# Optimization experiments

Hardware: AMD Instinct MI355X
Metric: run time of the kernel (lower is better)

Reference implementation:

```python
import jax, jax.numpy as jnp
import numpy as np
from jax import lax


def _maxpool_same(x, k):
    # stride-1 max pool with symmetric padding p=(k-1)//2, pad value -inf
    # (matches torch max_pool2d implicit -inf padding)
    p = (k - 1) // 2
    return lax.reduce_window(
        x,
        -jnp.inf,
        lax.max,
        window_dimensions=(1, 1, k, k),
        window_strides=(1, 1, 1, 1),
        padding=[(0, 0), (0, 0), (p, p), (p, p)],
    )


def setup_inputs() -> dict:
    key = jax.random.key(0)
    x = jax.random.normal(key, (16, 256, 64, 64), dtype=jnp.float32)
    return {"x": x}


def reference(x):
    # SPP: concat(x, maxpool5(x), maxpool9(x), maxpool13(x)) along channels
    x1 = _maxpool_same(x, 5)
    x2 = _maxpool_same(x, 9)
    x3 = _maxpool_same(x, 13)
    return jnp.concatenate([x, x1, x2, x3], axis=1)  # [B, 4C, H, W]
```

## Files before the change

### kernel.cpp

```cpp
#include <hip/hip_runtime.h>
#include <math.h>

#define TPB 256
#define W 64
#define H 64
#define LDSW 68

__global__ __launch_bounds__(TPB) void spp_kernel(const float* __restrict__ in,
                                                  float* __restrict__ out) {
    __shared__ __align__(16) float s_in[H * LDSW];
    __shared__ __align__(16) float s_r5[H * LDSW];
    __shared__ __align__(16) float s_r9[H * LDSW];
    __shared__ __align__(16) float s_r13[H * LDSW];

    const int tid = threadIdx.x;
    const int bc  = blockIdx.x;
    const int b   = bc >> 8;
    const int c   = bc & 255;
    const size_t img   = (size_t)bc * (H * W);
    const size_t obase = ((size_t)b * 1024 + c) * (H * W);
    const size_t pstr  = (size_t)256 * H * W;
    const float NEG = -INFINITY;

    {
        const float4* in4 = (const float4*)(in + img);
        #pragma unroll
        for (int i = 0; i < 4; ++i) {
            int idx = tid + TPB * i;
            int y = idx >> 4;
            int q = idx & 15;
            float4 v = in4[idx];
            *(float4*)&s_in[y * LDSW + q * 4] = v;
        }
    }
    __syncthreads();

    {
        const int y  = tid >> 2;
        const int x0 = (tid & 3) << 4;
        float seg[32];
        #pragma unroll
        for (int j = 0; j < 8; ++j) {
            int xs = x0 - 8 + 4 * j;
            float4 v;
            if (xs >= 0 && xs < W) v = *(const float4*)&s_in[y * LDSW + xs];
            else                   v = make_float4(NEG, NEG, NEG, NEG);
            seg[4*j+0] = v.x; seg[4*j+1] = v.y; seg[4*j+2] = v.z; seg[4*j+3] = v.w;
        }
        float r5[24];
        #pragma unroll
        for (int i = 0; i < 24; ++i) {
            float m = seg[i+2];
            m = fmaxf(m, seg[i+3]); m = fmaxf(m, seg[i+4]);
            m = fmaxf(m, seg[i+5]); m = fmaxf(m, seg[i+6]);
            r5[i] = m;
        }
        float r9[16], r13[16];
        #pragma unroll
        for (int i = 0; i < 16; ++i) {
            r9[i]  = fmaxf(r5[i+2], r5[i+6]);
            r13[i] = fmaxf(fmaxf(r5[i], r5[i+4]), r5[i+8]);
        }
        const int base = y * LDSW + x0;
        #pragma unroll
        for (int g = 0; g < 4; ++g) {
            *(float4*)&s_r5 [base + 4*g] = make_float4(r5[4+4*g], r5[5+4*g], r5[6+4*g], r5[7+4*g]);
            *(float4*)&s_r9 [base + 4*g] = make_float4(r9[4*g],  r9[4*g+1],  r9[4*g+2],  r9[4*g+3]);
            *(float4*)&s_r13[base + 4*g] = make_float4(r13[4*g], r13[4*g+1], r13[4*g+2], r13[4*g+3]);
        }
    }
    __syncthreads();

    {
        float4* o4 = (float4*)(out + obase);
        #pragma unroll
        for (int i = 0; i < 4; ++i) {
            int idx = tid + TPB * i;
            int y = idx >> 4;
            int q = idx & 15;
            o4[idx] = *(const float4*)&s_in[y * LDSW + q * 4];
        }
    }

    {
        const int x  = tid & 63;
        const int y0 = (tid >> 6) << 4;

        {
            float cv[20];
            #pragma unroll
            for (int j = 0; j < 20; ++j) {
                int y = y0 - 2 + j;
                cv[j] = (y >= 0 && y < H) ? s_r5[y * LDSW + x] : NEG;
            }
            float* o = out + obase + pstr;
            #pragma unroll
            for (int i = 0; i < 16; ++i) {
                float m = cv[i];
                m = fmaxf(m, cv[i+1]); m = fmaxf(m, cv[i+2]);
                m = fmaxf(m, cv[i+3]); m = fmaxf(m, cv[i+4]);
                o[(y0 + i) * W + x] = m;
            }
        }
        {
            float cv[24];
            #pragma unroll
            for (int j = 0; j < 24; ++j) {
                int y = y0 - 4 + j;
                cv[j] = (y >= 0 && y < H) ? s_r9[y * LDSW + x] : NEG;
            }
            float* o = out + obase + 2 * pstr;
            #pragma unroll
            for (int i = 0; i < 16; ++i) {
                float m = cv[i];
                #pragma unroll
                for (int d = 1; d < 9; ++d) m = fmaxf(m, cv[i+d]);
                o[(y0 + i) * W + x] = m;
            }
        }
        {
            float cv[28];
            #pragma unroll
            for (int j = 0; j < 28; ++j) {
                int y = y0 - 6 + j;
                cv[j] = (y >= 0 && y < H) ? s_r13[y * LDSW + x] : NEG;
            }
            float* o = out + obase + 3 * pstr;
            #pragma unroll
            for (int i = 0; i < 16; ++i) {
                float m = cv[i];
                #pragma unroll
                for (int d = 1; d < 13; ++d) m = fmaxf(m, cv[i+d]);
                o[(y0 + i) * W + x] = m;
            }
        }
    }
}

extern "C" void kernel_launch(void* const* d_in, const int* in_sizes, int n_in,
                              void* d_out, int out_size, void* d_ws, size_t ws_size,
                              hipStream_t stream) {
    const float* x = (const float*)d_in[0];
    float* out = (float*)d_out;
    spp_kernel<<<dim3(4096), dim3(TPB), 0, stream>>>(x, out);
}
```

Measured before the change: 315.3 us.

## Compute pyramid pooling from one horizontal-5 LDS buffer with wave shuffles

The kernel now computes the horizontal 5-wide max directly from global loads using wavefront shuffles, writes the passthrough channel straight from registers, and keeps only one LDS buffer instead of four. The vertical pass builds a prefix tree of pairwise maxima to get the 5, 9 and 13 vertical windows, then finishes the wider horizontal windows with cross-lane shuffles at offsets of 2 and 4, clamping at the image edges. This removes a full LDS staging pass, one barrier and three quarters of the LDS footprint, which should raise occupancy. In exchange it adds shuffle instructions and relies on the max-decomposition identities and edge clamping being correct.

```diff
diff --git a/kernel.cpp b/kernel.cpp
--- a/kernel.cpp
+++ b/kernel.cpp
@@ -8,15 +8,13 @@
 
 __global__ __launch_bounds__(TPB) void spp_kernel(const float* __restrict__ in,
                                                   float* __restrict__ out) {
-    __shared__ __align__(16) float s_in[H * LDSW];
     __shared__ __align__(16) float s_r5[H * LDSW];
-    __shared__ __align__(16) float s_r9[H * LDSW];
-    __shared__ __align__(16) float s_r13[H * LDSW];
 
-    const int tid = threadIdx.x;
-    const int bc  = blockIdx.x;
-    const int b   = bc >> 8;
-    const int c   = bc & 255;
+    const int tid  = threadIdx.x;
+    const int lane = tid & 63;
+    const int bc   = blockIdx.x;
+    const int b    = bc >> 8;
+    const int c    = bc & 255;
     const size_t img   = (size_t)bc * (H * W);
     const size_t obase = ((size_t)b * 1024 + c) * (H * W);
     const size_t pstr  = (size_t)256 * H * W;
@@ -24,115 +22,77 @@
 
     {
         const float4* in4 = (const float4*)(in + img);
+        float4* o4 = (float4*)(out + obase);
+        const int  lm1 = (lane - 1) & 63;
+        const int  lp1 = (lane + 1) & 63;
+        const bool qlo = (lane & 15) == 0;
+        const bool qhi = (lane & 15) == 15;
         #pragma unroll
         for (int i = 0; i < 4; ++i) {
-            int idx = tid + TPB * i;
-            int y = idx >> 4;
-            int q = idx & 15;
+            const int idx = tid + TPB * i;
             float4 v = in4[idx];
-            *(float4*)&s_in[y * LDSW + q * 4] = v;
+            o4[idx] = v;
+            float e0 = __shfl(v.z, lm1, 64);
+            float e1 = __shfl(v.w, lm1, 64);
+            float e6 = __shfl(v.x, lp1, 64);
+            float e7 = __shfl(v.y, lp1, 64);
+            if (qlo) { e0 = NEG; e1 = NEG; }
+            if (qhi) { e6 = NEG; e7 = NEG; }
+            const float e2 = v.x, e3 = v.y, e4 = v.z, e5 = v.w;
+            const float p0 = fmaxf(e0, e1), p1 = fmaxf(e1, e2), p2 = fmaxf(e2, e3);
+            const float p3 = fmaxf(e3, e4), p4 = fmaxf(e4, e5), p5 = fmaxf(e5, e6);
+            float4 r;
+            r.x = fmaxf(fmaxf(p0, p2), e4);
+            r.y = fmaxf(fmaxf(p1, p3), e5);
+            r.z = fmaxf(fmaxf(p2, p4), e6);
+            r.w = fmaxf(fmaxf(p3, p5), e7);
+            const int y = idx >> 4;
+            const int q = idx & 15;
+            *(float4*)&s_r5[y * LDSW + 4 * q] = r;
         }
     }
     __syncthreads();
 
     {
-        const int y  = tid >> 2;
-        const int x0 = (tid & 3) << 4;
-        float seg[32];
+        const int x  = lane;
+        const int y0 = (tid >> 6) << 4;
+        float cv[28];
         #pragma unroll
-        for (int j = 0; j < 8; ++j) {
-            int xs = x0 - 8 + 4 * j;
-            float4 v;
-            if (xs >= 0 && xs < W) v = *(const float4*)&s_in[y * LDSW + xs];
-            else                   v = make_float4(NEG, NEG, NEG, NEG);
-            seg[4*j+0] = v.x; seg[4*j+1] = v.y; seg[4*j+2] = v.z; seg[4*j+3] = v.w;
+        for (int j = 0; j < 28; ++j) {
+            const int y = y0 - 6 + j;
+            cv[j] = (y >= 0 && y < H) ? s_r5[y * LDSW + x] : NEG;
         }
-        float r5[24];
+        float p2a[27], p4a[25], p8a[21];
         #pragma unroll
-        for (int i = 0; i < 24; ++i) {
-            float m = seg[i+2];
-            m = fmaxf(m, seg[i+3]); m = fmaxf(m, seg[i+4]);
-            m = fmaxf(m, seg[i+5]); m = fmaxf(m, seg[i+6]);
-            r5[i] = m;
-        }
-        float r9[16], r13[16];
+        for (int j = 0; j < 27; ++j) p2a[j] = fmaxf(cv[j], cv[j + 1]);
+        #pragma unroll
+        for (int j = 0; j < 25; ++j) p4a[j] = fmaxf(p2a[j], p2a[j + 2]);
+        #pragma unroll
+        for (int j = 0; j < 21; ++j) p8a[j] = fmaxf(p4a[j], p4a[j + 4]);
+
+        const int xm2 = (x >= 2)  ? x - 2 : 0;
+        const int xp2 = (x <= 61) ? x + 2 : 63;
+        const int xm4 = (x >= 4)  ? x - 4 : 0;
+        const int xp4 = (x <= 59) ? x + 4 : 63;
+
+        float* o5  = out + obase +     pstr + x;
+        float* o9  = out + obase + 2 * pstr + x;
+        float* o13 = out + obase + 3 * pstr + x;
         #pragma unroll
         for (int i = 0; i < 16; ++i) {
-            r9[i]  = fmaxf(r5[i+2], r5[i+6]);
-            r13[i] = fmaxf(fmaxf(r5[i], r5[i+4]), r5[i+8]);
-        }
-        const int base = y * LDSW + x0;
-        #pragma unroll
-        for (int g = 0; g < 4; ++g) {
-            *(float4*)&s_r5 [base + 4*g] = make_float4(r5[4+4*g], r5[5+4*g], r5[6+4*g], r5[7+4*g]);
-            *(float4*)&s_r9 [base + 4*g] = make_float4(r9[4*g],  r9[4*g+1],  r9[4*g+2],  r9[4*g+3]);
-            *(float4*)&s_r13[base + 4*g] = make_float4(r13[4*g], r13[4*g+1], r13[4*g+2], r13[4*g+3]);
-        }
-    }
-    __syncthreads();
+            const float c5  = fmaxf(p4a[i + 4], cv[i + 8]);
+            const float c9  = fmaxf(p8a[i + 2], cv[i + 10]);
+            const float c13 = fmaxf(p8a[i], fmaxf(p4a[i + 8], cv[i + 12]));
 
-    {
-        float4* o4 = (float4*)(out + obase);
-        #pragma unroll
-        for (int i = 0; i < 4; ++i) {
-            int idx = tid + TPB * i;
-            int y = idx >> 4;
-            int q = idx & 15;
-            o4[idx] = *(const float4*)&s_in[y * LDSW + q * 4];
-        }
-    }
+            o5[(y0 + i) * W] = c5;
 
-    {
-        const int x  = tid & 63;
-        const int y0 = (tid >> 6) << 4;
+            const float a9 = __shfl(c9, xm2, 64);
+            const float b9 = __shfl(c9, xp2, 64);
+            o9[(y0 + i) * W] = fmaxf(a9, b9);
 
-        {
-            float cv[20];
-            #pragma unroll
-            for (int j = 0; j < 20; ++j) {
-                int y = y0 - 2 + j;
-                cv[j] = (y >= 0 && y < H) ? s_r5[y * LDSW + x] : NEG;
-            }
-            float* o = out + obase + pstr;
-            #pragma unroll
-            for (int i = 0; i < 16; ++i) {
-                float m = cv[i];
-                m = fmaxf(m, cv[i+1]); m = fmaxf(m, cv[i+2]);
-                m = fmaxf(m, cv[i+3]); m = fmaxf(m, cv[i+4]);
-                o[(y0 + i) * W + x] = m;
-            }
-        }
-        {
-            float cv[24];
-            #pragma unroll
-            for (int j = 0; j < 24; ++j) {
-                int y = y0 - 4 + j;
-                cv[j] = (y >= 0 && y < H) ? s_r9[y * LDSW + x] : NEG;
-            }
-            float* o = out + obase + 2 * pstr;
-            #pragma unroll
-            for (int i = 0; i < 16; ++i) {
-                float m = cv[i];
-                #pragma unroll
-                for (int d = 1; d < 9; ++d) m = fmaxf(m, cv[i+d]);
-                o[(y0 + i) * W + x] = m;
-            }
-        }
-        {
-            float cv[28];
-            #pragma unroll
-            for (int j = 0; j < 28; ++j) {
-                int y = y0 - 6 + j;
-                cv[j] = (y >= 0 && y < H) ? s_r13[y * LDSW + x] : NEG;
-            }
-            float* o = out + obase + 3 * pstr;
-            #pragma unroll
-            for (int i = 0; i < 16; ++i) {
-                float m = cv[i];
-                #pragma unroll
-                for (int d = 1; d < 13; ++d) m = fmaxf(m, cv[i+d]);
-                o[(y0 + i) * W + x] = m;
-            }
+            const float a13 = __shfl(c13, xm4, 64);
+            const float b13 = __shfl(c13, xp4, 64);
+            o13[(y0 + i) * W] = fmaxf(fmaxf(a13, c13), b13);
         }
     }
 }
```

After: 312.1 us. About the same (-1.0%).
